# Kernel optimization log

Hardware: AMD Instinct MI355X
Metric: run time of the kernel (lower is better)

## Reference

```python
import jax, jax.numpy as jnp
import numpy as np

KERNEL_SIZE = 4  # kernel_size=4, dim=1, degree-1 open B-splines (SplineConv defaults)


def spline_conv(x, edge_index, edge_attr, W, root, bias):
    """SplineConv with dim=1, kernel_size=4, degree=1, open splines, aggr='mean'.

    x: [N, F_in]; edge_index: [2, E] (row 0 = source, row 1 = target);
    edge_attr: [E, 1] pseudo-coords in [0,1]; W: [K, F_in, F_out];
    root: [F_in, F_out]; bias: [F_out].
    """
    N = x.shape[0]
    src, dst = edge_index[0], edge_index[1]
    u = edge_attr[:, 0]                          # [E]
    v = u * (KERNEL_SIZE - 1)                    # open spline: scale by K-1
    vf = jnp.floor(v)
    frac = v - vf                                # [E], degree-1 basis fraction
    k0 = jnp.clip(vf.astype(jnp.int32), 0, KERNEL_SIZE - 1)
    k1 = jnp.minimum(k0 + 1, KERNEL_SIZE - 1)
    # Project node features through all K kernel weights once: [N, K, F_out]
    xw = jnp.einsum('nf,kfo->nko', x, W)
    # Per-edge message: basis-weighted mix of the two active kernel projections
    m = (1.0 - frac)[:, None] * xw[src, k0] + frac[:, None] * xw[src, k1]  # [E, F_out]
    # Mean aggregation at target nodes
    agg = jax.ops.segment_sum(m, dst, num_segments=N)               # [N, F_out]
    deg = jax.ops.segment_sum(jnp.ones_like(u), dst, num_segments=N)
    agg = agg / jnp.maximum(deg, 1.0)[:, None]
    return agg + x @ root + bias


def setup_inputs() -> dict:
    key = jax.random.key(0)
    ks = jax.random.split(key, 9)
    N, E, F_IN, HID, C = 50000, 1600000, 48, 32, 10
    x = jax.random.normal(ks[0], (N, F_IN), dtype=jnp.float32)
    edge_index = jax.random.randint(ks[1], (2, E), 0, N, dtype=jnp.int64)
    edge_attr = jax.random.uniform(ks[2], (E, 1), dtype=jnp.float32)
    s = 0.1
    W1 = jax.random.normal(ks[3], (KERNEL_SIZE, F_IN, HID), dtype=jnp.float32) * s
    root1 = jax.random.normal(ks[4], (F_IN, HID), dtype=jnp.float32) * s
    bias1 = jax.random.normal(ks[5], (HID,), dtype=jnp.float32) * s
    W2 = jax.random.normal(ks[6], (KERNEL_SIZE, HID, C), dtype=jnp.float32) * s
    root2 = jax.random.normal(ks[7], (HID, C), dtype=jnp.float32) * s
    bias2 = jax.random.normal(ks[8], (C,), dtype=jnp.float32) * s
    return {"x": x, "edge_index": edge_index, "edge_attr": edge_attr,
            "W1": W1, "root1": root1, "bias1": bias1,
            "W2": W2, "root2": root2, "bias2": bias2}


def reference(x, edge_index, edge_attr, W1, root1, bias1, W2, root2, bias2):
    # dropout is identity in eval mode (training=self.training)
    h = spline_conv(x, edge_index, edge_attr, W1, root1, bias1)
    h = jax.nn.elu(h)
    h = spline_conv(h, edge_index, edge_attr, W2, root2, bias2)
    return jax.nn.log_softmax(h, axis=1)
```

## Files before the change

kernel.cpp:

```cpp
#include <hip/hip_runtime.h>
#include <math.h>


#define F_IN   48
#define HID    32
#define NCLS   10
#define KS     4
#define BKT_SH 8
#define TILE   4096

__device__ inline unsigned short f2bf(float f) {
    unsigned x = __float_as_uint(f);
    unsigned r = x + 0x7FFFu + ((x >> 16) & 1u);
    return (unsigned short)(r >> 16);
}
__device__ inline float bf2f(unsigned short u) {
    return __uint_as_float(((unsigned)u) << 16);
}


__global__ void bucket_hist_kernel(const int* __restrict__ ei, int* __restrict__ bcnt,
                                   int E, int NB) {
    __shared__ int lcnt[256];
    int t = threadIdx.x;
    lcnt[t] = 0;
    __syncthreads();
    int e0 = blockIdx.x * TILE;
    int n = min(TILE, E - e0);
    for (int r = 0; r < TILE / 256; ++r) {
        int i = r * 256 + t;
        if (i < n) atomicAdd(&lcnt[ei[E + e0 + i] >> BKT_SH], 1);
    }
    __syncthreads();
    if (t < NB && lcnt[t] > 0) atomicAdd(&bcnt[t], lcnt[t]);
}

__global__ void mini_scan_kernel(const int* __restrict__ bcnt, int* __restrict__ bbase,
                                 int* __restrict__ gcur, int NB) {
    __shared__ int a[256], c[256];
    int t = threadIdx.x;
    int v = (t < NB) ? bcnt[t] : 0;
    a[t] = v; c[t] = v;
    __syncthreads();
    for (int o = 1; o < 256; o <<= 1) {
        int w = (t >= o) ? a[t - o] : 0;
        __syncthreads();
        a[t] += w;
        __syncthreads();
    }
    int ex = a[t] - c[t];
    if (t < NB) { bbase[t] = ex; gcur[t] = ex; }
    if (t == 0) bbase[NB] = a[255];
}

__global__ void bucket_scatter_kernel(const int* __restrict__ ei, const float* __restrict__ ea,
                                      int* __restrict__ gcur, uint2* __restrict__ tpd,
                                      int E, int NB) {
    __shared__ unsigned spl[TILE];
    __shared__ unsigned short sdst[TILE];
    __shared__ unsigned short inv[TILE];
    __shared__ int lcnt[256], loff[256], lrank[256], gb[256];
    int t = threadIdx.x;
    lcnt[t] = 0; lrank[t] = 0;
    __syncthreads();
    int e0 = blockIdx.x * TILE;
    int n = min(TILE, E - e0);
    for (int r = 0; r < TILE / 256; ++r) {
        int i = r * 256 + t;
        if (i < n) {
            int e = e0 + i;
            int src = ei[e];
            int dst = ei[E + e];
            float u = ea[e];
            float v = u * (float)(KS - 1);
            float vf = floorf(v);
            int k0 = min(max((int)vf, 0), KS - 1);
            unsigned qf = (unsigned)((v - vf) * 16383.f + 0.5f);
            spl[i] = (unsigned)src | ((unsigned)k0 << 16) | (qf << 18);
            sdst[i] = (unsigned short)dst;
            atomicAdd(&lcnt[dst >> BKT_SH], 1);
        }
    }
    __syncthreads();
    loff[t] = lcnt[t];
    __syncthreads();
    for (int o = 1; o < 256; o <<= 1) {
        int w = (t >= o) ? loff[t - o] : 0;
        __syncthreads();
        loff[t] += w;
        __syncthreads();
    }
    int ex = loff[t] - lcnt[t];
    __syncthreads();
    loff[t] = ex;
    if (t < NB) gb[t] = atomicAdd(&gcur[t], lcnt[t]);
    __syncthreads();
    for (int r = 0; r < TILE / 256; ++r) {
        int i = r * 256 + t;
        if (i < n) {
            int b = sdst[i] >> BKT_SH;
            int p = loff[b] + atomicAdd(&lrank[b], 1);
            inv[p] = (unsigned short)i;
        }
    }
    __syncthreads();
    for (int r = 0; r < TILE / 256; ++r) {
        int j = r * 256 + t;
        if (j < n) {
            int i = inv[j];
            int d = sdst[i];
            int b = d >> BKT_SH;
            int pos = gb[b] + (j - loff[b]);
            tpd[pos] = make_uint2(spl[i], (unsigned)d);
        }
    }
}

__global__ void node_sort_kernel(const uint2* __restrict__ tpd, const int* __restrict__ bbase,
                                 unsigned* __restrict__ spk, int* __restrict__ offs,
                                 int N, int NB) {
    __shared__ int hc[256], hs[256], hr[256];
    int b = blockIdx.x;
    int t = threadIdx.x;
    int nb0 = b << BKT_SH;
    int nb = min(256, N - nb0);
    int base = bbase[b];
    int m = bbase[b + 1] - base;
    hc[t] = 0; hr[t] = 0;
    __syncthreads();
    for (int i = t; i < m; i += 256) atomicAdd(&hc[tpd[base + i].y - nb0], 1);
    __syncthreads();
    hs[t] = hc[t];
    __syncthreads();
    for (int o = 1; o < 256; o <<= 1) {
        int w = (t >= o) ? hs[t - o] : 0;
        __syncthreads();
        hs[t] += w;
        __syncthreads();
    }
    if (t < nb) offs[nb0 + t] = base + (hs[t] - hc[t]);
    if (b == NB - 1 && t == 0) offs[N] = base + m;
    for (int i = t; i < m; i += 256) {
        uint2 rec = tpd[base + i];
        int d = rec.y - nb0;
        int p = (hs[d] - hc[d]) + atomicAdd(&hr[d], 1);
        spk[base + p] = rec.x;
    }
}


__global__ __launch_bounds__(320) void xw1_kernel(
        const float* __restrict__ X, const float* __restrict__ W,
        const float* __restrict__ R, unsigned short* __restrict__ outk,
        float* __restrict__ outr, int n) {
    __shared__ float lw[48 * 160];
    int t = threadIdx.x;
    for (int i = t; i < 48 * 160; i += 320) {
        int f = i / 160;
        int col = i - f * 160;
        lw[i] = (col < 128) ? W[(size_t)(col >> 5) * (48 * 32) + f * 32 + (col & 31)]
                            : R[f * 32 + (col - 128)];
    }
    __syncthreads();
    int g = t % 40;
    int lp = t / 40;
    int n0 = (blockIdx.x * 8 + lp) * 2;
    if (n0 + 1 >= n) return;
    const float4* X0 = (const float4*)(X + (size_t)n0 * F_IN);
    const float4* X1 = (const float4*)(X + (size_t)(n0 + 1) * F_IN);
    float4 x0[12], x1[12];
#pragma unroll
    for (int i = 0; i < 12; ++i) { x0[i] = X0[i]; x1[i] = X1[i]; }
    const float4* lw4 = (const float4*)lw;
    float4 a0 = {0,0,0,0}, a1 = {0,0,0,0};
#pragma unroll
    for (int fb = 0; fb < 12; ++fb) {
        float4 v0 = x0[fb], v1 = x1[fb];
#pragma unroll
        for (int j = 0; j < 4; ++j) {
            float s0 = (j == 0) ? v0.x : (j == 1) ? v0.y : (j == 2) ? v0.z : v0.w;
            float s1 = (j == 0) ? v1.x : (j == 1) ? v1.y : (j == 2) ? v1.z : v1.w;
            float4 w = lw4[(fb * 4 + j) * 40 + g];
            a0.x = fmaf(s0, w.x, a0.x); a0.y = fmaf(s0, w.y, a0.y);
            a0.z = fmaf(s0, w.z, a0.z); a0.w = fmaf(s0, w.w, a0.w);
            a1.x = fmaf(s1, w.x, a1.x); a1.y = fmaf(s1, w.y, a1.y);
            a1.z = fmaf(s1, w.z, a1.z); a1.w = fmaf(s1, w.w, a1.w);
        }
    }
    if (g < 32) {
        uint2 u0, u1;
        u0.x = f2bf(a0.x) | ((unsigned)f2bf(a0.y) << 16);
        u0.y = f2bf(a0.z) | ((unsigned)f2bf(a0.w) << 16);
        u1.x = f2bf(a1.x) | ((unsigned)f2bf(a1.y) << 16);
        u1.y = f2bf(a1.z) | ((unsigned)f2bf(a1.w) << 16);
        *(uint2*)(outk + (size_t)n0 * (KS * HID) + g * 4) = u0;
        *(uint2*)(outk + (size_t)(n0 + 1) * (KS * HID) + g * 4) = u1;
    } else {
        int o = 4 * g - 128;
        *(float4*)(outr + (size_t)n0 * HID + o) = a0;
        *(float4*)(outr + (size_t)(n0 + 1) * HID + o) = a1;
    }
}

__global__ void xw2_kernel(const float* __restrict__ H, const float* __restrict__ W,
                           const float* __restrict__ R, unsigned short* __restrict__ outk,
                           float* __restrict__ outr, int n) {
    __shared__ float lw2[32 * 50];
    int t = threadIdx.x;
    for (int i = t; i < 32 * 50; i += 256) {
        int f = i / 50;
        int col = i - f * 50;
        lw2[i] = (col < 40) ? W[(size_t)(col / 10) * (32 * 10) + f * 10 + (col % 10)]
                            : R[f * 10 + (col - 40)];
    }
    __syncthreads();
    int total = (n / 2) * 25;
    int id = blockIdx.x * blockDim.x + t;
    if (id >= total) return;
    int p = id % 25;
    int pr = id / 25;
    int n0 = 2 * pr;
    const float4* H0 = (const float4*)(H + (size_t)n0 * HID);
    const float4* H1 = (const float4*)(H + (size_t)(n0 + 1) * HID);
    float4 h0[8], h1[8];
#pragma unroll
    for (int i = 0; i < 8; ++i) { h0[i] = H0[i]; h1[i] = H1[i]; }
    const float2* lwp = (const float2*)lw2;
    float ax0 = 0.f, ay0 = 0.f, ax1 = 0.f, ay1 = 0.f;
#pragma unroll
    for (int fb = 0; fb < 8; ++fb) {
        float4 v0 = h0[fb], v1 = h1[fb];
#pragma unroll
        for (int j = 0; j < 4; ++j) {
            float s0 = (j == 0) ? v0.x : (j == 1) ? v0.y : (j == 2) ? v0.z : v0.w;
            float s1 = (j == 0) ? v1.x : (j == 1) ? v1.y : (j == 2) ? v1.z : v1.w;
            float2 w = lwp[(fb * 4 + j) * 25 + p];
            ax0 = fmaf(s0, w.x, ax0); ay0 = fmaf(s0, w.y, ay0);
            ax1 = fmaf(s1, w.x, ax1); ay1 = fmaf(s1, w.y, ay1);
        }
    }
    int col = 2 * p;
    if (col < KS * NCLS) {
        *(unsigned*)(outk + (size_t)n0 * (KS * NCLS) + col) =
            f2bf(ax0) | ((unsigned)f2bf(ay0) << 16);
        *(unsigned*)(outk + (size_t)(n0 + 1) * (KS * NCLS) + col) =
            f2bf(ax1) | ((unsigned)f2bf(ay1) << 16);
    } else {
        int o = col - KS * NCLS;
        *(float2*)(outr + (size_t)n0 * NCLS + o) = make_float2(ax0, ay0);
        *(float2*)(outr + (size_t)(n0 + 1) * NCLS + o) = make_float2(ax1, ay1);
    }
}


__device__ inline float interp32(const unsigned short* __restrict__ xwk, unsigned p, int c) {
    int src = p & 0xFFFF;
    int k0 = (p >> 16) & 3;
    int k1 = min(k0 + 1, KS - 1);
    float fr = (float)(p >> 18) * (1.f / 16383.f);
    const unsigned short* row = xwk + (size_t)src * (KS * HID);
    float v0 = bf2f(row[k0 * HID + c]);
    float v1 = bf2f(row[k1 * HID + c]);
    return fmaf(fr, v1 - v0, v0);
}

__global__ void agg1_kernel(const unsigned short* __restrict__ xwk,
                            const float* __restrict__ xroot,
                            const int* __restrict__ offs, const unsigned* __restrict__ spk,
                            const float* __restrict__ bias, float* __restrict__ h, int n) {
    int c = threadIdx.x & 31;
    int node = blockIdx.x * 8 + (threadIdx.x >> 5);
    if (node >= n) return;
    int beg = offs[node];
    int end = offs[node + 1];
    float s0 = 0.f, s1 = 0.f;
    int e = beg;
    for (; e + 2 <= end; e += 2) {
        unsigned p0 = spk[e];
        unsigned p1 = spk[e + 1];
        s0 += interp32(xwk, p0, c);
        s1 += interp32(xwk, p1, c);
    }
    if (e < end) s0 += interp32(xwk, spk[e], c);
    float sum = s0 + s1;
    int deg = end - beg;
    float m = sum / (float)(deg > 0 ? deg : 1);
    float o = m + xroot[(size_t)node * HID + c] + bias[c];
    h[(size_t)node * HID + c] = (o > 0.f) ? o : expm1f(o);
}

__device__ inline float interp10(const unsigned short* __restrict__ xwk, unsigned p, int cc) {
    int src = p & 0xFFFF;
    int k0 = (p >> 16) & 3;
    int k1 = min(k0 + 1, KS - 1);
    float fr = (float)(p >> 18) * (1.f / 16383.f);
    const unsigned short* row = xwk + (size_t)src * (KS * NCLS);
    float v0 = bf2f(row[k0 * NCLS + cc]);
    float v1 = bf2f(row[k1 * NCLS + cc]);
    return fmaf(fr, v1 - v0, v0);
}

__global__ void agg2_kernel(const unsigned short* __restrict__ xwk,
                            const float* __restrict__ xroot,
                            const int* __restrict__ offs, const unsigned* __restrict__ spk,
                            const float* __restrict__ bias, float* __restrict__ out, int n) {
    int c = threadIdx.x & 15;
    int node = blockIdx.x * 16 + (threadIdx.x >> 4);
    if (node >= n) return;
    int cc = min(c, NCLS - 1);
    int beg = offs[node];
    int end = offs[node + 1];
    float s0 = 0.f, s1 = 0.f;
    int e = beg;
    for (; e + 2 <= end; e += 2) {
        unsigned p0 = spk[e];
        unsigned p1 = spk[e + 1];
        s0 += interp10(xwk, p0, cc);
        s1 += interp10(xwk, p1, cc);
    }
    if (e < end) s0 += interp10(xwk, spk[e], cc);
    float sum = s0 + s1;
    int deg = end - beg;
    float m = sum / (float)(deg > 0 ? deg : 1);
    float logit = m + xroot[(size_t)node * NCLS + cc] + bias[cc];
    bool active = (c < NCLS);
    float mx = active ? logit : -INFINITY;
#pragma unroll
    for (int msk = 1; msk < 16; msk <<= 1) mx = fmaxf(mx, __shfl_xor(mx, msk, 16));
    float ex = active ? expf(logit - mx) : 0.f;
    float s = ex;
#pragma unroll
    for (int msk = 1; msk < 16; msk <<= 1) s += __shfl_xor(s, msk, 16);
    if (active) out[(size_t)node * NCLS + c] = (logit - mx) - logf(s);
}

extern "C" void kernel_launch(void* const* d_in, const int* in_sizes, int n_in,
                              void* d_out, int out_size, void* d_ws, size_t ws_size,
                              hipStream_t stream) {
    const float* x       = (const float*)d_in[0];
    const int*   ei      = (const int*)d_in[1];
    const float* ea      = (const float*)d_in[2];
    const float* W1      = (const float*)d_in[3];
    const float* root1   = (const float*)d_in[4];
    const float* bias1   = (const float*)d_in[5];
    const float* W2      = (const float*)d_in[6];
    const float* root2   = (const float*)d_in[7];
    const float* bias2   = (const float*)d_in[8];
    float* out = (float*)d_out;

    const int N = in_sizes[0] / F_IN;
    const int E = in_sizes[2];
    const int NB = (N + 255) >> BKT_SH;

    char* base = (char*)d_ws;
    size_t off = 0;
    auto alloc = [&](size_t bytes) {
        char* p = base + off;
        off = (off + bytes + 255) & ~(size_t)255;
        return (void*)p;
    };
    unsigned short* xwk1 = (unsigned short*)alloc((size_t)N * KS * HID * 2);
    float* xr1           = (float*)alloc((size_t)N * HID * 4);
    float* h             = (float*)alloc((size_t)N * HID * 4);
    int* offs            = (int*)alloc(((size_t)N + 1) * 4);
    int* bcnt            = (int*)alloc((size_t)NB * 4);
    int* bbase           = (int*)alloc(((size_t)NB + 1) * 4);
    int* gcur            = (int*)alloc((size_t)NB * 4);
    unsigned* spk        = (unsigned*)alloc((size_t)E * 4);
    uint2* tpd           = (uint2*)xwk1;
    unsigned short* xwk2 = xwk1;
    float* xr2           = xr1;
    if (ws_size < off) return;

    int ebk = (E + TILE - 1) / TILE;

    hipMemsetAsync(bcnt, 0, (size_t)NB * 4, stream);
    bucket_hist_kernel<<<ebk, 256, 0, stream>>>(ei, bcnt, E, NB);
    mini_scan_kernel<<<1, 256, 0, stream>>>(bcnt, bbase, gcur, NB);
    bucket_scatter_kernel<<<ebk, 256, 0, stream>>>(ei, ea, gcur, tpd, E, NB);
    node_sort_kernel<<<NB, 256, 0, stream>>>(tpd, bbase, spk, offs, N, NB);
    xw1_kernel<<<(N + 15) / 16, 320, 0, stream>>>(x, W1, root1, xwk1, xr1, N);
    agg1_kernel<<<(N + 7) / 8, 256, 0, stream>>>(xwk1, xr1, offs, spk, bias1, h, N);
    {
        int total = (N / 2) * 25;
        xw2_kernel<<<(total + 255) / 256, 256, 0, stream>>>(h, W2, root2, xwk2, xr2, N);
    }
    agg2_kernel<<<(N + 15) / 16, 256, 0, stream>>>(xwk2, xr2, offs, spk, bias2, out, N);
}
```

Measured before the change: 271.3 us.

## Split projected feature tables into 8-channel quarter planes for cache-local gathers

Both projection tables and the hidden/root buffers are moved to a blocked layout: the channels are split into groups of 8, each stored as its own contiguous plane of 16-byte rows per (node, kernel). The edge record now packs src*4+k0, so a single index addresses k0 and k1 as adjacent rows. Aggregation kernels give each block one channel group and spread 8 edges across lanes, then reduce with shuffles. Log-softmax moves into a separate kernel. The intent is a smaller, cache-friendly working set per gather pass, at the cost of re-reading the edge list once per channel group and one extra launch.

```diff
diff --git a/kernel.cpp b/kernel.cpp
--- a/kernel.cpp
+++ b/kernel.cpp
@@ -76,7 +76,7 @@
             float vf = floorf(v);
             int k0 = min(max((int)vf, 0), KS - 1);
             unsigned qf = (unsigned)((v - vf) * 16383.f + 0.5f);
-            spl[i] = (unsigned)src | ((unsigned)k0 << 16) | (qf << 18);
+            spl[i] = ((unsigned)src << 2) | (unsigned)k0 | (qf << 18);
             sdst[i] = (unsigned short)dst;
             atomicAdd(&lcnt[dst >> BKT_SH], 1);
         }
@@ -152,7 +152,7 @@
 __global__ __launch_bounds__(320) void xw1_kernel(
         const float* __restrict__ X, const float* __restrict__ W,
         const float* __restrict__ R, unsigned short* __restrict__ outk,
-        float* __restrict__ outr, int n) {
+        float* __restrict__ outr, int n, int qsk, int qsf) {
     __shared__ float lw[48 * 160];
     int t = threadIdx.x;
     for (int i = t; i < 48 * 160; i += 320) {
@@ -188,23 +188,31 @@
         }
     }
     if (g < 32) {
+        int k = g >> 3;
+        int c0 = (g & 7) * 4;
+        int q = c0 >> 3;
+        int coff = c0 & 7;
         uint2 u0, u1;
         u0.x = f2bf(a0.x) | ((unsigned)f2bf(a0.y) << 16);
         u0.y = f2bf(a0.z) | ((unsigned)f2bf(a0.w) << 16);
         u1.x = f2bf(a1.x) | ((unsigned)f2bf(a1.y) << 16);
         u1.y = f2bf(a1.z) | ((unsigned)f2bf(a1.w) << 16);
-        *(uint2*)(outk + (size_t)n0 * (KS * HID) + g * 4) = u0;
-        *(uint2*)(outk + (size_t)(n0 + 1) * (KS * HID) + g * 4) = u1;
+        size_t bi = (size_t)q * qsk + (size_t)k * 8 + coff;
+        *(uint2*)(outk + bi + (size_t)n0 * 32) = u0;
+        *(uint2*)(outk + bi + (size_t)(n0 + 1) * 32) = u1;
     } else {
-        int o = 4 * g - 128;
-        *(float4*)(outr + (size_t)n0 * HID + o) = a0;
-        *(float4*)(outr + (size_t)(n0 + 1) * HID + o) = a1;
+        int o = (g - 32) * 4;
+        int q = o >> 3;
+        int coff = o & 7;
+        size_t bi = (size_t)q * qsf + coff;
+        *(float4*)(outr + bi + (size_t)n0 * 8) = a0;
+        *(float4*)(outr + bi + (size_t)(n0 + 1) * 8) = a1;
     }
 }
 
 __global__ void xw2_kernel(const float* __restrict__ H, const float* __restrict__ W,
                            const float* __restrict__ R, unsigned short* __restrict__ outk,
-                           float* __restrict__ outr, int n) {
+                           float* __restrict__ outr, int n, int hqs, int qsk, int qsf) {
     __shared__ float lw2[32 * 50];
     int t = threadIdx.x;
     for (int i = t; i < 32 * 50; i += 256) {
@@ -220,11 +228,14 @@
     int p = id % 25;
     int pr = id / 25;
     int n0 = 2 * pr;
-    const float4* H0 = (const float4*)(H + (size_t)n0 * HID);
-    const float4* H1 = (const float4*)(H + (size_t)(n0 + 1) * HID);
     float4 h0[8], h1[8];
 #pragma unroll
-    for (int i = 0; i < 8; ++i) { h0[i] = H0[i]; h1[i] = H1[i]; }
+    for (int qq = 0; qq < 4; ++qq) {
+        const float4* Hq0 = (const float4*)(H + (size_t)qq * hqs + (size_t)n0 * 8);
+        const float4* Hq1 = (const float4*)(H + (size_t)qq * hqs + (size_t)(n0 + 1) * 8);
+        h0[qq * 2] = Hq0[0]; h0[qq * 2 + 1] = Hq0[1];
+        h1[qq * 2] = Hq1[0]; h1[qq * 2 + 1] = Hq1[1];
+    }
     const float2* lwp = (const float2*)lw2;
     float ax0 = 0.f, ay0 = 0.f, ax1 = 0.f, ay1 = 0.f;
 #pragma unroll
@@ -240,98 +251,124 @@
         }
     }
     int col = 2 * p;
-    if (col < KS * NCLS) {
-        *(unsigned*)(outk + (size_t)n0 * (KS * NCLS) + col) =
+    if (col < 40) {
+        int k = col / 10;
+        int o = col - k * 10;
+        int hf = o >> 3;
+        int coff = o & 7;
+        size_t bi = (size_t)hf * qsk + (size_t)k * 8 + coff;
+        *(unsigned*)(outk + bi + (size_t)n0 * 32) =
             f2bf(ax0) | ((unsigned)f2bf(ay0) << 16);
-        *(unsigned*)(outk + (size_t)(n0 + 1) * (KS * NCLS) + col) =
+        *(unsigned*)(outk + bi + (size_t)(n0 + 1) * 32) =
             f2bf(ax1) | ((unsigned)f2bf(ay1) << 16);
     } else {
-        int o = col - KS * NCLS;
-        *(float2*)(outr + (size_t)n0 * NCLS + o) = make_float2(ax0, ay0);
-        *(float2*)(outr + (size_t)(n0 + 1) * NCLS + o) = make_float2(ax1, ay1);
-    }
-}
-
-
-__device__ inline float interp32(const unsigned short* __restrict__ xwk, unsigned p, int c) {
-    int src = p & 0xFFFF;
-    int k0 = (p >> 16) & 3;
-    int k1 = min(k0 + 1, KS - 1);
+        int o = col - 40;
+        int hf = o >> 3;
+        int coff = o & 7;
+        size_t bi = (size_t)hf * qsf + coff;
+        *(float2*)(outr + bi + (size_t)n0 * 8) = make_float2(ax0, ay0);
+        *(float2*)(outr + bi + (size_t)(n0 + 1) * 8) = make_float2(ax1, ay1);
+    }
+}
+
+
+__device__ inline float gath(const unsigned short* __restrict__ tbl, unsigned p) {
+    unsigned sk = p & 0x3FFFFu;
     float fr = (float)(p >> 18) * (1.f / 16383.f);
-    const unsigned short* row = xwk + (size_t)src * (KS * HID);
-    float v0 = bf2f(row[k0 * HID + c]);
-    float v1 = bf2f(row[k1 * HID + c]);
+    float v0 = bf2f(tbl[sk * 8]);
+    float v1 = bf2f(tbl[sk * 8 + 8]);
     return fmaf(fr, v1 - v0, v0);
 }
 
 __global__ void agg1_kernel(const unsigned short* __restrict__ xwk,
                             const float* __restrict__ xroot,
                             const int* __restrict__ offs, const unsigned* __restrict__ spk,
-                            const float* __restrict__ bias, float* __restrict__ h, int n) {
-    int c = threadIdx.x & 31;
-    int node = blockIdx.x * 8 + (threadIdx.x >> 5);
+                            const float* __restrict__ bias, float* __restrict__ h,
+                            int n, int qsk, int qsf) {
+    int lane = threadIdx.x & 63;
+    int slot = lane >> 3;
+    int c = lane & 7;
+    int q = blockIdx.x & 3;
+    int node = (blockIdx.x >> 2) * 4 + (threadIdx.x >> 6);
     if (node >= n) return;
-    int beg = offs[node];
-    int end = offs[node + 1];
+    const unsigned short* tbl = xwk + (size_t)q * qsk + c;
+    int beg = offs[node], end = offs[node + 1];
     float s0 = 0.f, s1 = 0.f;
-    int e = beg;
-    for (; e + 2 <= end; e += 2) {
-        unsigned p0 = spk[e];
-        unsigned p1 = spk[e + 1];
-        s0 += interp32(xwk, p0, c);
-        s1 += interp32(xwk, p1, c);
-    }
-    if (e < end) s0 += interp32(xwk, spk[e], c);
+    int e = beg + slot;
+    for (; e + 8 < end; e += 16) {
+        unsigned p0 = __builtin_nontemporal_load(spk + e);
+        unsigned p1 = __builtin_nontemporal_load(spk + e + 8);
+        s0 += gath(tbl, p0);
+        s1 += gath(tbl, p1);
+    }
+    if (e < end) s0 += gath(tbl, __builtin_nontemporal_load(spk + e));
     float sum = s0 + s1;
-    int deg = end - beg;
-    float m = sum / (float)(deg > 0 ? deg : 1);
-    float o = m + xroot[(size_t)node * HID + c] + bias[c];
-    h[(size_t)node * HID + c] = (o > 0.f) ? o : expm1f(o);
-}
-
-__device__ inline float interp10(const unsigned short* __restrict__ xwk, unsigned p, int cc) {
-    int src = p & 0xFFFF;
-    int k0 = (p >> 16) & 3;
-    int k1 = min(k0 + 1, KS - 1);
-    float fr = (float)(p >> 18) * (1.f / 16383.f);
-    const unsigned short* row = xwk + (size_t)src * (KS * NCLS);
-    float v0 = bf2f(row[k0 * NCLS + cc]);
-    float v1 = bf2f(row[k1 * NCLS + cc]);
-    return fmaf(fr, v1 - v0, v0);
+    sum += __shfl_xor(sum, 8, 64);
+    sum += __shfl_xor(sum, 16, 64);
+    sum += __shfl_xor(sum, 32, 64);
+    if (slot == 0) {
+        int deg = end - beg;
+        float m = sum / (float)(deg > 0 ? deg : 1);
+        size_t idx = (size_t)q * qsf + (size_t)node * 8 + c;
+        float o = m + xroot[idx] + bias[q * 8 + c];
+        h[idx] = (o > 0.f) ? o : expm1f(o);
+    }
 }
 
 __global__ void agg2_kernel(const unsigned short* __restrict__ xwk,
                             const float* __restrict__ xroot,
                             const int* __restrict__ offs, const unsigned* __restrict__ spk,
-                            const float* __restrict__ bias, float* __restrict__ out, int n) {
-    int c = threadIdx.x & 15;
-    int node = blockIdx.x * 16 + (threadIdx.x >> 4);
+                            const float* __restrict__ bias, float* __restrict__ lg,
+                            int n, int qsk, int qsf) {
+    int lane = threadIdx.x & 63;
+    int slot = lane >> 3;
+    int c = lane & 7;
+    int hf = blockIdx.x & 1;
+    int node = (blockIdx.x >> 1) * 4 + (threadIdx.x >> 6);
     if (node >= n) return;
-    int cc = min(c, NCLS - 1);
-    int beg = offs[node];
-    int end = offs[node + 1];
+    const unsigned short* tbl = xwk + (size_t)hf * qsk + c;
+    int beg = offs[node], end = offs[node + 1];
     float s0 = 0.f, s1 = 0.f;
-    int e = beg;
-    for (; e + 2 <= end; e += 2) {
-        unsigned p0 = spk[e];
-        unsigned p1 = spk[e + 1];
-        s0 += interp10(xwk, p0, cc);
-        s1 += interp10(xwk, p1, cc);
-    }
-    if (e < end) s0 += interp10(xwk, spk[e], cc);
+    int e = beg + slot;
+    for (; e + 8 < end; e += 16) {
+        unsigned p0 = __builtin_nontemporal_load(spk + e);
+        unsigned p1 = __builtin_nontemporal_load(spk + e + 8);
+        s0 += gath(tbl, p0);
+        s1 += gath(tbl, p1);
+    }
+    if (e < end) s0 += gath(tbl, __builtin_nontemporal_load(spk + e));
     float sum = s0 + s1;
-    int deg = end - beg;
-    float m = sum / (float)(deg > 0 ? deg : 1);
-    float logit = m + xroot[(size_t)node * NCLS + cc] + bias[cc];
-    bool active = (c < NCLS);
-    float mx = active ? logit : -INFINITY;
-#pragma unroll
-    for (int msk = 1; msk < 16; msk <<= 1) mx = fmaxf(mx, __shfl_xor(mx, msk, 16));
-    float ex = active ? expf(logit - mx) : 0.f;
-    float s = ex;
-#pragma unroll
-    for (int msk = 1; msk < 16; msk <<= 1) s += __shfl_xor(s, msk, 16);
-    if (active) out[(size_t)node * NCLS + c] = (logit - mx) - logf(s);
+    sum += __shfl_xor(sum, 8, 64);
+    sum += __shfl_xor(sum, 16, 64);
+    sum += __shfl_xor(sum, 32, 64);
+    if (slot == 0) {
+        int deg = end - beg;
+        float m = sum / (float)(deg > 0 ? deg : 1);
+        size_t idx = (size_t)hf * qsf + (size_t)node * 8 + c;
+        int ch = hf * 8 + c;
+        lg[idx] = m + xroot[idx] + bias[min(ch, NCLS - 1)];
+    }
+}
+
+__global__ void softmax_kernel(const float* __restrict__ lg, float* __restrict__ out,
+                               int n, int qsf) {
+    int i = blockIdx.x * 256 + threadIdx.x;
+    if (i >= n) return;
+    const float* l0 = lg + (size_t)i * 8;
+    float4 a = *(const float4*)l0;
+    float4 b = *(const float4*)(l0 + 4);
+    float2 cp = *(const float2*)(lg + (size_t)qsf + (size_t)i * 8);
+    float v[10] = {a.x, a.y, a.z, a.w, b.x, b.y, b.z, b.w, cp.x, cp.y};
+    float mx = v[0];
+#pragma unroll
+    for (int j = 1; j < 10; ++j) mx = fmaxf(mx, v[j]);
+    float s = 0.f;
+#pragma unroll
+    for (int j = 0; j < 10; ++j) s += expf(v[j] - mx);
+    float ls = logf(s) + mx;
+    float* o = out + (size_t)i * 10;
+#pragma unroll
+    for (int j = 0; j < 10; ++j) o[j] = v[j] - ls;
 }
 
 extern "C" void kernel_launch(void* const* d_in, const int* in_sizes, int n_in,
@@ -351,6 +388,8 @@
     const int N = in_sizes[0] / F_IN;
     const int E = in_sizes[2];
     const int NB = (N + 255) >> BKT_SH;
+    const int QSK = (N + 1) * 32;
+    const int QSF = N * 8;
 
     char* base = (char*)d_ws;
     size_t off = 0;
@@ -359,9 +398,9 @@
         off = (off + bytes + 255) & ~(size_t)255;
         return (void*)p;
     };
-    unsigned short* xwk1 = (unsigned short*)alloc((size_t)N * KS * HID * 2);
-    float* xr1           = (float*)alloc((size_t)N * HID * 4);
-    float* h             = (float*)alloc((size_t)N * HID * 4);
+    unsigned short* xwk1 = (unsigned short*)alloc((size_t)4 * QSK * 2);
+    float* xr1           = (float*)alloc((size_t)4 * QSF * 4);
+    float* h             = (float*)alloc((size_t)4 * QSF * 4);
     int* offs            = (int*)alloc(((size_t)N + 1) * 4);
     int* bcnt            = (int*)alloc((size_t)NB * 4);
     int* bbase           = (int*)alloc(((size_t)NB + 1) * 4);
@@ -370,6 +409,7 @@
     uint2* tpd           = (uint2*)xwk1;
     unsigned short* xwk2 = xwk1;
     float* xr2           = xr1;
+    float* lg            = h;
     if (ws_size < off) return;
 
     int ebk = (E + TILE - 1) / TILE;
@@ -379,11 +419,15 @@
     mini_scan_kernel<<<1, 256, 0, stream>>>(bcnt, bbase, gcur, NB);
     bucket_scatter_kernel<<<ebk, 256, 0, stream>>>(ei, ea, gcur, tpd, E, NB);
     node_sort_kernel<<<NB, 256, 0, stream>>>(tpd, bbase, spk, offs, N, NB);
-    xw1_kernel<<<(N + 15) / 16, 320, 0, stream>>>(x, W1, root1, xwk1, xr1, N);
-    agg1_kernel<<<(N + 7) / 8, 256, 0, stream>>>(xwk1, xr1, offs, spk, bias1, h, N);
+    xw1_kernel<<<(N + 15) / 16, 320, 0, stream>>>(x, W1, root1, xwk1, xr1, N, QSK, QSF);
+    agg1_kernel<<<((N + 3) / 4) * 4, 256, 0, stream>>>(xwk1, xr1, offs, spk, bias1, h,
+                                                       N, QSK, QSF);
     {
         int total = (N / 2) * 25;
-        xw2_kernel<<<(total + 255) / 256, 256, 0, stream>>>(h, W2, root2, xwk2, xr2, N);
-    }
-    agg2_kernel<<<(N + 15) / 16, 256, 0, stream>>>(xwk2, xr2, offs, spk, bias2, out, N);
-}
+        xw2_kernel<<<(total + 255) / 256, 256, 0, stream>>>(h, W2, root2, xwk2, xr2,
+                                                            N, QSF, QSK, QSF);
+    }
+    agg2_kernel<<<((N + 3) / 4) * 2, 256, 0, stream>>>(xwk2, xr2, offs, spk, bias2, lg,
+                                                       N, QSK, QSF);
+    softmax_kernel<<<(N + 255) / 256, 256, 0, stream>>>(lg, out, N, QSF);
+}
```

Result: slower. 326.7 us (+20.4%).

## Partition edges by source quarter across blocks and split aggregation with atomic accumulators

Applied to the files above, without the earlier changes.

Node sort now bins each target's edges by which quarter of the source-node range they come from, producing per-node-per-quarter offsets. The aggregation kernels launch one block group per quarter, so concurrently running blocks gather from a smaller source window, aiming for better L2/cache locality. Each quarter atomically adds partial sums into zeroed accumulators, and separate finalize kernels apply the mean, root, bias and activation or log_softmax. The packed edge word and the layer-2 table padding are changed so the gather index is a single mask. The cost is extra memsets, atomics, two more launches and more workspace.

```diff
diff --git a/kernel.cpp b/kernel.cpp
--- a/kernel.cpp
+++ b/kernel.cpp
@@ -76,7 +76,7 @@
             float vf = floorf(v);
             int k0 = min(max((int)vf, 0), KS - 1);
             unsigned qf = (unsigned)((v - vf) * 16383.f + 0.5f);
-            spl[i] = (unsigned)src | ((unsigned)k0 << 16) | (qf << 18);
+            spl[i] = ((unsigned)src << 2) | (unsigned)k0 | (qf << 18);
             sdst[i] = (unsigned short)dst;
             atomicAdd(&lcnt[dst >> BKT_SH], 1);
         }
@@ -117,34 +117,48 @@
 }
 
 __global__ void node_sort_kernel(const uint2* __restrict__ tpd, const int* __restrict__ bbase,
-                                 unsigned* __restrict__ spk, int* __restrict__ offs,
-                                 int N, int NB) {
-    __shared__ int hc[256], hs[256], hr[256];
+                                 unsigned* __restrict__ spk, int* __restrict__ offs4,
+                                 int N, int NB, int Q) {
+    __shared__ int hc[1024], hs[1024], hr[1024], part[256];
     int b = blockIdx.x;
     int t = threadIdx.x;
     int nb0 = b << BKT_SH;
     int nb = min(256, N - nb0);
     int base = bbase[b];
     int m = bbase[b + 1] - base;
-    hc[t] = 0; hr[t] = 0;
-    __syncthreads();
-    for (int i = t; i < m; i += 256) atomicAdd(&hc[tpd[base + i].y - nb0], 1);
-    __syncthreads();
-    hs[t] = hc[t];
+    for (int j = t; j < 1024; j += 256) { hc[j] = 0; hr[j] = 0; }
+    __syncthreads();
+    for (int i = t; i < m; i += 256) {
+        uint2 r = tpd[base + i];
+        int d = r.y - nb0;
+        int src = (r.x >> 2) & 0xFFFF;
+        int qt = (src >= Q) + (src >= 2 * Q) + (src >= 3 * Q);
+        atomicAdd(&hc[(d << 2) | qt], 1);
+    }
+    __syncthreads();
+    int s = hc[4 * t] + hc[4 * t + 1] + hc[4 * t + 2] + hc[4 * t + 3];
+    part[t] = s;
     __syncthreads();
     for (int o = 1; o < 256; o <<= 1) {
-        int w = (t >= o) ? hs[t - o] : 0;
-        __syncthreads();
-        hs[t] += w;
-        __syncthreads();
-    }
-    if (t < nb) offs[nb0 + t] = base + (hs[t] - hc[t]);
-    if (b == NB - 1 && t == 0) offs[N] = base + m;
+        int w = (t >= o) ? part[t - o] : 0;
+        __syncthreads();
+        part[t] += w;
+        __syncthreads();
+    }
+    int run = part[t] - s;
+#pragma unroll
+    for (int j = 0; j < 4; ++j) { hs[4 * t + j] = run; run += hc[4 * t + j]; }
+    __syncthreads();
+    for (int j = t; j < 4 * nb; j += 256) offs4[(nb0 << 2) + j] = base + hs[j];
+    if (b == NB - 1 && t == 0) offs4[4 * N] = base + m;
     for (int i = t; i < m; i += 256) {
-        uint2 rec = tpd[base + i];
-        int d = rec.y - nb0;
-        int p = (hs[d] - hc[d]) + atomicAdd(&hr[d], 1);
-        spk[base + p] = rec.x;
+        uint2 r = tpd[base + i];
+        int d = r.y - nb0;
+        int src = (r.x >> 2) & 0xFFFF;
+        int qt = (src >= Q) + (src >= 2 * Q) + (src >= 3 * Q);
+        int bin = (d << 2) | qt;
+        int p = hs[bin] + atomicAdd(&hr[bin], 1);
+        spk[base + p] = r.x;
     }
 }
 
@@ -240,98 +254,127 @@
         }
     }
     int col = 2 * p;
-    if (col < KS * NCLS) {
-        *(unsigned*)(outk + (size_t)n0 * (KS * NCLS) + col) =
+    if (col < 40) {
+        int k = col / 10;
+        int o = col - k * 10;
+        *(unsigned*)(outk + (size_t)n0 * 64 + k * 16 + o) =
             f2bf(ax0) | ((unsigned)f2bf(ay0) << 16);
-        *(unsigned*)(outk + (size_t)(n0 + 1) * (KS * NCLS) + col) =
+        *(unsigned*)(outk + (size_t)(n0 + 1) * 64 + k * 16 + o) =
             f2bf(ax1) | ((unsigned)f2bf(ay1) << 16);
     } else {
-        int o = col - KS * NCLS;
+        int o = col - 40;
         *(float2*)(outr + (size_t)n0 * NCLS + o) = make_float2(ax0, ay0);
         *(float2*)(outr + (size_t)(n0 + 1) * NCLS + o) = make_float2(ax1, ay1);
     }
 }
 
 
-__device__ inline float interp32(const unsigned short* __restrict__ xwk, unsigned p, int c) {
-    int src = p & 0xFFFF;
-    int k0 = (p >> 16) & 3;
-    int k1 = min(k0 + 1, KS - 1);
+__device__ inline float g32(const unsigned short* __restrict__ tbl, unsigned p) {
+    unsigned sk = p & 0x3FFFFu;
     float fr = (float)(p >> 18) * (1.f / 16383.f);
-    const unsigned short* row = xwk + (size_t)src * (KS * HID);
-    float v0 = bf2f(row[k0 * HID + c]);
-    float v1 = bf2f(row[k1 * HID + c]);
+    float v0 = bf2f(tbl[sk * 32]);
+    float v1 = bf2f(tbl[sk * 32 + 32]);
     return fmaf(fr, v1 - v0, v0);
 }
 
 __global__ void agg1_kernel(const unsigned short* __restrict__ xwk,
-                            const float* __restrict__ xroot,
-                            const int* __restrict__ offs, const unsigned* __restrict__ spk,
-                            const float* __restrict__ bias, float* __restrict__ h, int n) {
-    int c = threadIdx.x & 31;
-    int node = blockIdx.x * 8 + (threadIdx.x >> 5);
+                            const int* __restrict__ offs4, const unsigned* __restrict__ spk,
+                            float* __restrict__ hacc, int n) {
+    int lane = threadIdx.x & 63;
+    int c = lane & 31;
+    int slot = lane >> 5;
+    int qt = blockIdx.x & 3;
+    int node = (blockIdx.x >> 2) * 4 + (threadIdx.x >> 6);
     if (node >= n) return;
-    int beg = offs[node];
-    int end = offs[node + 1];
+    int beg = offs4[node * 4 + qt], end = offs4[node * 4 + qt + 1];
+    if (beg == end) return;
+    const unsigned short* tbl = xwk + c;
     float s0 = 0.f, s1 = 0.f;
-    int e = beg;
-    for (; e + 2 <= end; e += 2) {
-        unsigned p0 = spk[e];
-        unsigned p1 = spk[e + 1];
-        s0 += interp32(xwk, p0, c);
-        s1 += interp32(xwk, p1, c);
-    }
-    if (e < end) s0 += interp32(xwk, spk[e], c);
+    int e = beg + slot;
+    for (; e + 2 < end; e += 4) {
+        unsigned p0 = __builtin_nontemporal_load(spk + e);
+        unsigned p1 = __builtin_nontemporal_load(spk + e + 2);
+        s0 += g32(tbl, p0);
+        s1 += g32(tbl, p1);
+    }
+    if (e < end) s0 += g32(tbl, __builtin_nontemporal_load(spk + e));
     float sum = s0 + s1;
-    int deg = end - beg;
-    float m = sum / (float)(deg > 0 ? deg : 1);
-    float o = m + xroot[(size_t)node * HID + c] + bias[c];
-    h[(size_t)node * HID + c] = (o > 0.f) ? o : expm1f(o);
-}
-
-__device__ inline float interp10(const unsigned short* __restrict__ xwk, unsigned p, int cc) {
-    int src = p & 0xFFFF;
-    int k0 = (p >> 16) & 3;
-    int k1 = min(k0 + 1, KS - 1);
+    sum += __shfl_xor(sum, 32, 64);
+    if (slot == 0) atomicAdd(&hacc[(size_t)node * HID + c], sum);
+}
+
+__global__ void fin1_kernel(const float* __restrict__ hacc, const float* __restrict__ xr,
+                            const int* __restrict__ offs4, const float* __restrict__ bias,
+                            float* __restrict__ h, int n) {
+    int id = blockIdx.x * 256 + threadIdx.x;
+    if (id >= n * HID) return;
+    int node = id >> 5, c = id & 31;
+    int deg = offs4[node * 4 + 4] - offs4[node * 4];
+    float m = hacc[id] / (float)(deg > 0 ? deg : 1);
+    float o = m + xr[id] + bias[c];
+    h[id] = (o > 0.f) ? o : expm1f(o);
+}
+
+__device__ inline float g16(const unsigned short* __restrict__ tbl, unsigned p) {
+    unsigned sk = p & 0x3FFFFu;
     float fr = (float)(p >> 18) * (1.f / 16383.f);
-    const unsigned short* row = xwk + (size_t)src * (KS * NCLS);
-    float v0 = bf2f(row[k0 * NCLS + cc]);
-    float v1 = bf2f(row[k1 * NCLS + cc]);
+    float v0 = bf2f(tbl[sk * 16]);
+    float v1 = bf2f(tbl[sk * 16 + 16]);
     return fmaf(fr, v1 - v0, v0);
 }
 
 __global__ void agg2_kernel(const unsigned short* __restrict__ xwk,
-                            const float* __restrict__ xroot,
-                            const int* __restrict__ offs, const unsigned* __restrict__ spk,
-                            const float* __restrict__ bias, float* __restrict__ out, int n) {
-    int c = threadIdx.x & 15;
-    int node = blockIdx.x * 16 + (threadIdx.x >> 4);
+                            const int* __restrict__ offs4, const unsigned* __restrict__ spk,
+                            float* __restrict__ lacc, int n) {
+    int lane = threadIdx.x & 63;
+    int c = lane & 15;
+    int slot = lane >> 4;
+    int qt = blockIdx.x & 3;
+    int node = (blockIdx.x >> 2) * 4 + (threadIdx.x >> 6);
     if (node >= n) return;
-    int cc = min(c, NCLS - 1);
-    int beg = offs[node];
-    int end = offs[node + 1];
+    int beg = offs4[node * 4 + qt], end = offs4[node * 4 + qt + 1];
+    if (beg == end) return;
+    const unsigned short* tbl = xwk + c;
     float s0 = 0.f, s1 = 0.f;
-    int e = beg;
-    for (; e + 2 <= end; e += 2) {
-        unsigned p0 = spk[e];
-        unsigned p1 = spk[e + 1];
-        s0 += interp10(xwk, p0, cc);
-        s1 += interp10(xwk, p1, cc);
-    }
-    if (e < end) s0 += interp10(xwk, spk[e], cc);
+    int e = beg + slot;
+    for (; e + 4 < end; e += 8) {
+        unsigned p0 = __builtin_nontemporal_load(spk + e);
+        unsigned p1 = __builtin_nontemporal_load(spk + e + 4);
+        s0 += g16(tbl, p0);
+        s1 += g16(tbl, p1);
+    }
+    if (e < end) s0 += g16(tbl, __builtin_nontemporal_load(spk + e));
     float sum = s0 + s1;
-    int deg = end - beg;
-    float m = sum / (float)(deg > 0 ? deg : 1);
-    float logit = m + xroot[(size_t)node * NCLS + cc] + bias[cc];
-    bool active = (c < NCLS);
-    float mx = active ? logit : -INFINITY;
-#pragma unroll
-    for (int msk = 1; msk < 16; msk <<= 1) mx = fmaxf(mx, __shfl_xor(mx, msk, 16));
-    float ex = active ? expf(logit - mx) : 0.f;
-    float s = ex;
-#pragma unroll
-    for (int msk = 1; msk < 16; msk <<= 1) s += __shfl_xor(s, msk, 16);
-    if (active) out[(size_t)node * NCLS + c] = (logit - mx) - logf(s);
+    sum += __shfl_xor(sum, 16, 64);
+    sum += __shfl_xor(sum, 32, 64);
+    if (lane < 16) atomicAdd(&lacc[(size_t)node * 16 + c], sum);
+}
+
+__global__ void fin2_kernel(const float* __restrict__ lacc, const float* __restrict__ xr,
+                            const int* __restrict__ offs4, const float* __restrict__ bias,
+                            float* __restrict__ out, int n) {
+    int i = blockIdx.x * 256 + threadIdx.x;
+    if (i >= n) return;
+    int deg = offs4[i * 4 + 4] - offs4[i * 4];
+    float inv = 1.f / (float)(deg > 0 ? deg : 1);
+    const float* l0 = lacc + (size_t)i * 16;
+    float4 a = *(const float4*)l0;
+    float4 b = *(const float4*)(l0 + 4);
+    float2 cpair = *(const float2*)(l0 + 8);
+    float v[10] = {a.x, a.y, a.z, a.w, b.x, b.y, b.z, b.w, cpair.x, cpair.y};
+    const float* rr = xr + (size_t)i * NCLS;
+#pragma unroll
+    for (int j = 0; j < 10; ++j) v[j] = v[j] * inv + rr[j] + bias[j];
+    float mx = v[0];
+#pragma unroll
+    for (int j = 1; j < 10; ++j) mx = fmaxf(mx, v[j]);
+    float s = 0.f;
+#pragma unroll
+    for (int j = 0; j < 10; ++j) s += expf(v[j] - mx);
+    float ls = logf(s) + mx;
+    float* o = out + (size_t)i * 10;
+#pragma unroll
+    for (int j = 0; j < 10; ++j) o[j] = v[j] - ls;
 }
 
 extern "C" void kernel_launch(void* const* d_in, const int* in_sizes, int n_in,
@@ -351,6 +394,7 @@
     const int N = in_sizes[0] / F_IN;
     const int E = in_sizes[2];
     const int NB = (N + 255) >> BKT_SH;
+    const int Q  = (N + 3) / 4;
 
     char* base = (char*)d_ws;
     size_t off = 0;
@@ -359,31 +403,37 @@
         off = (off + bytes + 255) & ~(size_t)255;
         return (void*)p;
     };
-    unsigned short* xwk1 = (unsigned short*)alloc((size_t)N * KS * HID * 2);
+    unsigned short* xwk1 = (unsigned short*)alloc((size_t)N * 128 * 2);
     float* xr1           = (float*)alloc((size_t)N * HID * 4);
     float* h             = (float*)alloc((size_t)N * HID * 4);
-    int* offs            = (int*)alloc(((size_t)N + 1) * 4);
+    float* hacc          = (float*)alloc((size_t)N * HID * 4);
+    float* lacc          = (float*)alloc((size_t)N * 16 * 4);
+    float* xr2           = (float*)alloc((size_t)N * NCLS * 4);
+    int* offs4           = (int*)alloc(((size_t)4 * N + 1) * 4);
     int* bcnt            = (int*)alloc((size_t)NB * 4);
     int* bbase           = (int*)alloc(((size_t)NB + 1) * 4);
     int* gcur            = (int*)alloc((size_t)NB * 4);
     unsigned* spk        = (unsigned*)alloc((size_t)E * 4);
     uint2* tpd           = (uint2*)xwk1;
     unsigned short* xwk2 = xwk1;
-    float* xr2           = xr1;
     if (ws_size < off) return;
 
     int ebk = (E + TILE - 1) / TILE;
 
     hipMemsetAsync(bcnt, 0, (size_t)NB * 4, stream);
+    hipMemsetAsync(hacc, 0, (size_t)N * HID * 4, stream);
+    hipMemsetAsync(lacc, 0, (size_t)N * 16 * 4, stream);
     bucket_hist_kernel<<<ebk, 256, 0, stream>>>(ei, bcnt, E, NB);
     mini_scan_kernel<<<1, 256, 0, stream>>>(bcnt, bbase, gcur, NB);
     bucket_scatter_kernel<<<ebk, 256, 0, stream>>>(ei, ea, gcur, tpd, E, NB);
-    node_sort_kernel<<<NB, 256, 0, stream>>>(tpd, bbase, spk, offs, N, NB);
+    node_sort_kernel<<<NB, 256, 0, stream>>>(tpd, bbase, spk, offs4, N, NB, Q);
     xw1_kernel<<<(N + 15) / 16, 320, 0, stream>>>(x, W1, root1, xwk1, xr1, N);
-    agg1_kernel<<<(N + 7) / 8, 256, 0, stream>>>(xwk1, xr1, offs, spk, bias1, h, N);
+    agg1_kernel<<<((N + 3) / 4) * 4, 256, 0, stream>>>(xwk1, offs4, spk, hacc, N);
+    fin1_kernel<<<(N * HID + 255) / 256, 256, 0, stream>>>(hacc, xr1, offs4, bias1, h, N);
     {
         int total = (N / 2) * 25;
         xw2_kernel<<<(total + 255) / 256, 256, 0, stream>>>(h, W2, root2, xwk2, xr2, N);
     }
-    agg2_kernel<<<(N + 15) / 16, 256, 0, stream>>>(xwk2, xr2, offs, spk, bias2, out, N);
-}
+    agg2_kernel<<<((N + 3) / 4) * 4, 256, 0, stream>>>(xwk2, offs4, spk, lacc, N);
+    fin2_kernel<<<(N + 255) / 256, 256, 0, stream>>>(lacc, xr2, offs4, bias2, out, N);
+}
```

Result: slower. 349.0 us (+28.6%).
